# Performance work log

Hardware: AMD Instinct MI355X
Metric: run time of the kernel (lower is better)

## Reference

```python
import jax, jax.numpy as jnp
import numpy as np

LOCAL_SIZE = 20
SAMPLING_RATE = 10
LN_EPS = 1e-5


def _layer_norm(x, gamma, beta):
    m = x.mean(axis=-1, keepdims=True)
    v = ((x - m) ** 2).mean(axis=-1, keepdims=True)
    return (x - m) / jnp.sqrt(v + LN_EPS) * gamma + beta


def setup_inputs() -> dict:
    key = jax.random.key(0)
    ks = jax.random.split(key, 3)
    B, T, D, R = 32, 4096, 512, 64
    return {
        "obs_frames": jax.random.normal(ks[0], (B, T, D), dtype=jnp.float32),
        "w_red": (jax.random.normal(ks[1], (D, R), dtype=jnp.float32) / np.float32(np.sqrt(D))),
        "b_red": jnp.zeros((R,), jnp.float32),
        "g_red": jnp.ones((R,), jnp.float32),
        "beta_red": jnp.zeros((R,), jnp.float32),
        "w_exp": (jax.random.normal(ks[2], (R, D), dtype=jnp.float32) / np.float32(np.sqrt(R))),
        "b_exp": jnp.zeros((D,), jnp.float32),
        "g_exp": jnp.ones((D,), jnp.float32),
        "beta_exp": jnp.zeros((D,), jnp.float32),
    }


def reference(obs_frames, w_red, b_red, g_red, beta_red, w_exp, b_exp, g_exp, beta_exp):
    # linear_reduction: Linear -> ReLU -> LayerNorm, [B,T,D] -> [B,T,R]
    cf = _layer_norm(jax.nn.relu(jnp.einsum("btd,dr->btr", obs_frames, w_red) + b_red), g_red, beta_red)
    T = cf.shape[1]
    # max over strided past frames: indices 0, 10, ..., < T-LOCAL_SIZE
    past_pooled = jnp.max(cf[:, : T - LOCAL_SIZE : SAMPLING_RATE, :], axis=1)  # [B,R]
    # hand-rolled cummax over the last LOCAL_SIZE steps, seeded with past max
    present = cf[:, -LOCAL_SIZE:, :]                                           # [B,L,R]
    seeded = jnp.concatenate([past_pooled[:, None, :], present], axis=1)       # [B,L+1,R]
    global_reduc_max = jax.lax.associative_scan(jnp.maximum, seeded, axis=1)[:, 1:, :]  # [B,L,R]
    # _linear_expand: Linear -> ReLU -> LayerNorm, [B,L,R] -> [B,L,D]
    global_max = _layer_norm(jax.nn.relu(jnp.einsum("blr,rd->bld", global_reduc_max, w_exp) + b_exp), g_exp, beta_exp)
    now_reduc_max = cf[:, -1:, :]  # [B,1,R]
    return (global_max, now_reduc_max)
```

## Files before the change

kernel.cpp:

```cpp
#include <hip/hip_runtime.h>

static constexpr int Bsz   = 32;
static constexpr int Tlen  = 4096;
static constexpr int Ddim  = 512;
static constexpr int NSAMP = 408;
static constexpr int NPRES = 20;
static constexpr int NROWS = NSAMP + NPRES;
static constexpr int RPB   = 64;
static constexpr int NBLK  = 7;

typedef __attribute__((ext_vector_type(8))) short short8;
typedef __attribute__((ext_vector_type(4))) float f32x4;

__device__ __forceinline__ unsigned short f2bf(float x) {
  union { float f; unsigned u; } c; c.f = x;
  unsigned r = c.u + 0x7FFFu + ((c.u >> 16) & 1u);
  return (unsigned short)(r >> 16);
}

__device__ __forceinline__ int swz(int row, int colByte) {
  return (row << 10) + (colByte ^ ((row & 7) << 4));
}

__global__ __launch_bounds__(256) void k1_cf(
    const float* __restrict__ obs, const float* __restrict__ wred,
    const float* __restrict__ bred, const float* __restrict__ gred,
    const float* __restrict__ betared,
    float* __restrict__ bpart,
    float* __restrict__ present,
    float* __restrict__ out_now)
{
  __shared__ short xs[RPB * Ddim];
  __shared__ short wt[64 * Ddim];
  __shared__ float wmax[4][64];

  const int b    = blockIdx.y;
  const int bx   = blockIdx.x;
  const int base = bx * RPB;
  const int tid  = threadIdx.x;
  char* xsB = (char*)xs;
  char* wtB = (char*)wt;

  const float* obs_b = obs + (size_t)b * Tlen * Ddim;
#pragma unroll 8
  for (int it = 0; it < 32; ++it) {
    int u    = it * 256 + tid;
    int row  = u >> 7;
    int c4   = u & 127;
    int graw = base + row;
    int gr   = graw < NROWS ? graw : NROWS - 1;
    int t    = gr < NSAMP ? gr * 10 : (Tlen - NPRES) + (gr - NSAMP);
    float4 v = *(const float4*)(obs_b + (size_t)t * Ddim + c4 * 4);
    uint2 wv;
    wv.x = (unsigned)f2bf(v.x) | ((unsigned)f2bf(v.y) << 16);
    wv.y = (unsigned)f2bf(v.z) | ((unsigned)f2bf(v.w) << 16);
    *(uint2*)(xsB + swz(row, c4 * 8)) = wv;
  }

#pragma unroll 4
  for (int it = 0; it < 16; ++it) {
    int dp = it * 16 + (tid >> 4);
    int d  = dp * 2;
    int r0 = (tid & 15) * 4;
    float4 va = *(const float4*)(wred + (size_t)d * 64 + r0);
    float4 vb = *(const float4*)(wred + (size_t)(d + 1) * 64 + r0);
    *(unsigned*)(wtB + swz(r0 + 0, d * 2)) =
        (unsigned)f2bf(va.x) | ((unsigned)f2bf(vb.x) << 16);
    *(unsigned*)(wtB + swz(r0 + 1, d * 2)) =
        (unsigned)f2bf(va.y) | ((unsigned)f2bf(vb.y) << 16);
    *(unsigned*)(wtB + swz(r0 + 2, d * 2)) =
        (unsigned)f2bf(va.z) | ((unsigned)f2bf(vb.z) << 16);
    *(unsigned*)(wtB + swz(r0 + 3, d * 2)) =
        (unsigned)f2bf(va.w) | ((unsigned)f2bf(vb.w) << 16);
  }
  __syncthreads();

  const int w    = tid >> 6;
  const int lane = tid & 63;
  const int l15  = lane & 15;
  const int lhi  = lane >> 4;
  const int arow = w * 16 + l15;

  f32x4 acc0 = {0.f, 0.f, 0.f, 0.f};
  f32x4 acc1 = {0.f, 0.f, 0.f, 0.f};
  f32x4 acc2 = {0.f, 0.f, 0.f, 0.f};
  f32x4 acc3 = {0.f, 0.f, 0.f, 0.f};
#pragma unroll
  for (int ks = 0; ks < 16; ++ks) {
    int colB = ks * 64 + lhi * 16;
    short8 av  = *(const short8*)(xsB + swz(arow,     colB));
    short8 bv0 = *(const short8*)(wtB + swz(l15,      colB));
    short8 bv1 = *(const short8*)(wtB + swz(16 + l15, colB));
    short8 bv2 = *(const short8*)(wtB + swz(32 + l15, colB));
    short8 bv3 = *(const short8*)(wtB + swz(48 + l15, colB));
    acc0 = __builtin_amdgcn_mfma_f32_16x16x32_bf16(av, bv0, acc0, 0, 0, 0);
    acc1 = __builtin_amdgcn_mfma_f32_16x16x32_bf16(av, bv1, acc1, 0, 0, 0);
    acc2 = __builtin_amdgcn_mfma_f32_16x16x32_bf16(av, bv2, acc2, 0, 0, 0);
    acc3 = __builtin_amdgcn_mfma_f32_16x16x32_bf16(av, bv3, acc3, 0, 0, 0);
  }

  const int ch0 = l15, ch1 = 16 + l15, ch2 = 32 + l15, ch3 = 48 + l15;
  const float bb0 = bred[ch0], bb1 = bred[ch1], bb2 = bred[ch2], bb3 = bred[ch3];
  const float gg0 = gred[ch0], gg1 = gred[ch1], gg2 = gred[ch2], gg3 = gred[ch3];
  const float be0 = betared[ch0], be1 = betared[ch1];
  const float be2 = betared[ch2], be3 = betared[ch3];
  float m0 = -INFINITY, m1 = -INFINITY, m2 = -INFINITY, m3 = -INFINITY;
  float* pres_b = present + (size_t)b * NPRES * 64;

#pragma unroll
  for (int q = 0; q < 4; ++q) {
    int rloc = lhi * 4 + q;
    int graw = base + w * 16 + rloc;
    int gr   = graw < NROWS ? graw : NROWS - 1;
    float y0 = fmaxf(acc0[q] + bb0, 0.f);
    float y1 = fmaxf(acc1[q] + bb1, 0.f);
    float y2 = fmaxf(acc2[q] + bb2, 0.f);
    float y3 = fmaxf(acc3[q] + bb3, 0.f);
    float s  = y0 + y1 + y2 + y3;
    float s2 = y0 * y0 + y1 * y1 + y2 * y2 + y3 * y3;
#pragma unroll
    for (int msk = 1; msk <= 8; msk <<= 1) {
      s  += __shfl_xor(s,  msk, 64);
      s2 += __shfl_xor(s2, msk, 64);
    }
    float mean = s * (1.f / 64.f);
    float var  = s2 * (1.f / 64.f) - mean * mean;
    float inv  = rsqrtf(fmaxf(var, 0.f) + 1e-5f);
    float c0 = (y0 - mean) * inv * gg0 + be0;
    float c1 = (y1 - mean) * inv * gg1 + be1;
    float c2 = (y2 - mean) * inv * gg2 + be2;
    float c3 = (y3 - mean) * inv * gg3 + be3;
    if (gr < NSAMP) {
      m0 = fmaxf(m0, c0); m1 = fmaxf(m1, c1);
      m2 = fmaxf(m2, c2); m3 = fmaxf(m3, c3);
    } else {
      int l = gr - NSAMP;
      pres_b[l * 64 + ch0] = c0;  pres_b[l * 64 + ch1] = c1;
      pres_b[l * 64 + ch2] = c2;  pres_b[l * 64 + ch3] = c3;
      if (gr == NROWS - 1) {
        out_now[b * 64 + ch0] = c0;  out_now[b * 64 + ch1] = c1;
        out_now[b * 64 + ch2] = c2;  out_now[b * 64 + ch3] = c3;
      }
    }
  }

  m0 = fmaxf(m0, __shfl_xor(m0, 16, 64)); m0 = fmaxf(m0, __shfl_xor(m0, 32, 64));
  m1 = fmaxf(m1, __shfl_xor(m1, 16, 64)); m1 = fmaxf(m1, __shfl_xor(m1, 32, 64));
  m2 = fmaxf(m2, __shfl_xor(m2, 16, 64)); m2 = fmaxf(m2, __shfl_xor(m2, 32, 64));
  m3 = fmaxf(m3, __shfl_xor(m3, 16, 64)); m3 = fmaxf(m3, __shfl_xor(m3, 32, 64));
  if (lhi == 0) {
    wmax[w][ch0] = m0; wmax[w][ch1] = m1; wmax[w][ch2] = m2; wmax[w][ch3] = m3;
  }
  __syncthreads();
  if (tid < 64) {
    float m = fmaxf(fmaxf(wmax[0][tid], wmax[1][tid]),
                    fmaxf(wmax[2][tid], wmax[3][tid]));
    bpart[((size_t)b * NBLK + bx) * 64 + tid] = m;
  }
}

__global__ __launch_bounds__(256) void k3_expand(
    const float* __restrict__ wexp, const float* __restrict__ bexp,
    const float* __restrict__ gexp, const float* __restrict__ betaexp,
    const float* __restrict__ bpart, const float* __restrict__ present,
    float* __restrict__ out_gm)
{
  __shared__ float part[4][64];
  __shared__ float gm[64];
  __shared__ float red_s[4], red_s2[4];
  __shared__ float bc[2];
  const int l = blockIdx.x;
  const int b = blockIdx.y;
  const int tid = threadIdx.x;
  const int r = tid & 63, j = tid >> 6;

  const int nsrc = NBLK + l + 1;
  float v = -INFINITY;
  for (int s = j; s < nsrc; s += 4)
    v = fmaxf(v, s < NBLK ? bpart[((size_t)b * NBLK + s) * 64 + r]
                          : present[((size_t)b * NPRES + (s - NBLK)) * 64 + r]);
  part[j][r] = v;
  __syncthreads();
  if (tid < 64)
    gm[tid] = fmaxf(fmaxf(part[0][tid], part[1][tid]),
                    fmaxf(part[2][tid], part[3][tid]));
  __syncthreads();

  const int d0 = tid, d1 = tid + 256;
  float a0 = 0.f, a1 = 0.f;
#pragma unroll 8
  for (int rr = 0; rr < 64; ++rr) {
    float g = gm[rr];
    a0 = fmaf(g, wexp[rr * Ddim + d0], a0);
    a1 = fmaf(g, wexp[rr * Ddim + d1], a1);
  }
  float y0 = fmaxf(a0 + bexp[d0], 0.f);
  float y1 = fmaxf(a1 + bexp[d1], 0.f);

  float s = y0 + y1, s2 = fmaf(y0, y0, y1 * y1);
#pragma unroll
  for (int m = 32; m >= 1; m >>= 1) {
    s  += __shfl_xor(s,  m, 64);
    s2 += __shfl_xor(s2, m, 64);
  }
  int wid = tid >> 6, lane = tid & 63;
  if (lane == 0) { red_s[wid] = s; red_s2[wid] = s2; }
  __syncthreads();
  if (tid == 0) {
    float S  = red_s[0] + red_s[1] + red_s[2] + red_s[3];
    float S2 = red_s2[0] + red_s2[1] + red_s2[2] + red_s2[3];
    float mean = S * (1.f / 512.f);
    float var  = S2 * (1.f / 512.f) - mean * mean;
    bc[0] = mean;
    bc[1] = rsqrtf(fmaxf(var, 0.f) + 1e-5f);
  }
  __syncthreads();
  float mean = bc[0], inv = bc[1];
  size_t o = ((size_t)b * NPRES + l) * Ddim;
  out_gm[o + d0] = (y0 - mean) * inv * gexp[d0] + betaexp[d0];
  out_gm[o + d1] = (y1 - mean) * inv * gexp[d1] + betaexp[d1];
}

extern "C" void kernel_launch(void* const* d_in, const int* in_sizes, int n_in,
                              void* d_out, int out_size, void* d_ws, size_t ws_size,
                              hipStream_t stream) {
  const float* obs     = (const float*)d_in[0];
  const float* wred    = (const float*)d_in[1];
  const float* bred    = (const float*)d_in[2];
  const float* gred    = (const float*)d_in[3];
  const float* betared = (const float*)d_in[4];
  const float* wexp    = (const float*)d_in[5];
  const float* bexp    = (const float*)d_in[6];
  const float* gexp    = (const float*)d_in[7];
  const float* betaexp = (const float*)d_in[8];

  float* out_gm  = (float*)d_out;
  float* out_now = (float*)d_out + Bsz * NPRES * Ddim;

  float* bpart   = (float*)d_ws;
  float* present = bpart + Bsz * NBLK * 64;

  dim3 g1(NBLK, Bsz);
  k1_cf<<<g1, 256, 0, stream>>>(obs, wred, bred, gred, betared,
                                bpart, present, out_now);

  dim3 g3(NPRES, Bsz);
  k3_expand<<<g3, 256, 0, stream>>>(wexp, bexp, gexp, betaexp,
                                    bpart, present, out_gm);
}
```

Before: 26.38 us.

## Widen reduction kernel to 1024 threads and fuse two output rows per expand block

The first kernel now launches 1024 threads per block. Each of its 16 waves computes one 16x16 MFMA tile, split by row group and channel group, instead of 4 waves each computing four tiles. LayerNorm statistics are then combined across waves through shared memory, which adds a barrier. The aim is more memory-level parallelism for the strided gather of input frames, since only 224 blocks run. The expand kernel now handles two output time steps per block, reusing each loaded w_exp value for both rows and halving the grid.

```diff
diff --git a/kernel.cpp b/kernel.cpp
--- a/kernel.cpp
+++ b/kernel.cpp
@@ -22,7 +22,7 @@
   return (row << 10) + (colByte ^ ((row & 7) << 4));
 }
 
-__global__ __launch_bounds__(256) void k1_cf(
+__global__ __launch_bounds__(1024) void k1_cf(
     const float* __restrict__ obs, const float* __restrict__ wred,
     const float* __restrict__ bred, const float* __restrict__ gred,
     const float* __restrict__ betared,
@@ -32,6 +32,8 @@
 {
   __shared__ short xs[RPB * Ddim];
   __shared__ short wt[64 * Ddim];
+  __shared__ float sred[64][4];
+  __shared__ float s2red[64][4];
   __shared__ float wmax[4][64];
 
   const int b    = blockIdx.y;
@@ -42,9 +44,9 @@
   char* wtB = (char*)wt;
 
   const float* obs_b = obs + (size_t)b * Tlen * Ddim;
-#pragma unroll 8
-  for (int it = 0; it < 32; ++it) {
-    int u    = it * 256 + tid;
+#pragma unroll
+  for (int it = 0; it < 8; ++it) {
+    int u    = it * 1024 + tid;
     int row  = u >> 7;
     int c4   = u & 127;
     int graw = base + row;
@@ -57,9 +59,9 @@
     *(uint2*)(xsB + swz(row, c4 * 8)) = wv;
   }
 
-#pragma unroll 4
-  for (int it = 0; it < 16; ++it) {
-    int dp = it * 16 + (tid >> 4);
+#pragma unroll
+  for (int it = 0; it < 4; ++it) {
+    int dp = it * 64 + (tid >> 4);
     int d  = dp * 2;
     int r0 = (tid & 15) * 4;
     float4 va = *(const float4*)(wred + (size_t)d * 64 + r0);
@@ -79,83 +81,70 @@
   const int lane = tid & 63;
   const int l15  = lane & 15;
   const int lhi  = lane >> 4;
-  const int arow = w * 16 + l15;
-
-  f32x4 acc0 = {0.f, 0.f, 0.f, 0.f};
-  f32x4 acc1 = {0.f, 0.f, 0.f, 0.f};
-  f32x4 acc2 = {0.f, 0.f, 0.f, 0.f};
-  f32x4 acc3 = {0.f, 0.f, 0.f, 0.f};
+  const int rowg = w & 3;
+  const int chg  = w >> 2;
+  const int arow = rowg * 16 + l15;
+  const int brow = chg * 16 + l15;
+
+  f32x4 acc = {0.f, 0.f, 0.f, 0.f};
 #pragma unroll
   for (int ks = 0; ks < 16; ++ks) {
     int colB = ks * 64 + lhi * 16;
-    short8 av  = *(const short8*)(xsB + swz(arow,     colB));
-    short8 bv0 = *(const short8*)(wtB + swz(l15,      colB));
-    short8 bv1 = *(const short8*)(wtB + swz(16 + l15, colB));
-    short8 bv2 = *(const short8*)(wtB + swz(32 + l15, colB));
-    short8 bv3 = *(const short8*)(wtB + swz(48 + l15, colB));
-    acc0 = __builtin_amdgcn_mfma_f32_16x16x32_bf16(av, bv0, acc0, 0, 0, 0);
-    acc1 = __builtin_amdgcn_mfma_f32_16x16x32_bf16(av, bv1, acc1, 0, 0, 0);
-    acc2 = __builtin_amdgcn_mfma_f32_16x16x32_bf16(av, bv2, acc2, 0, 0, 0);
-    acc3 = __builtin_amdgcn_mfma_f32_16x16x32_bf16(av, bv3, acc3, 0, 0, 0);
-  }
-
-  const int ch0 = l15, ch1 = 16 + l15, ch2 = 32 + l15, ch3 = 48 + l15;
-  const float bb0 = bred[ch0], bb1 = bred[ch1], bb2 = bred[ch2], bb3 = bred[ch3];
-  const float gg0 = gred[ch0], gg1 = gred[ch1], gg2 = gred[ch2], gg3 = gred[ch3];
-  const float be0 = betared[ch0], be1 = betared[ch1];
-  const float be2 = betared[ch2], be3 = betared[ch3];
-  float m0 = -INFINITY, m1 = -INFINITY, m2 = -INFINITY, m3 = -INFINITY;
-  float* pres_b = present + (size_t)b * NPRES * 64;
-
+    short8 av = *(const short8*)(xsB + swz(arow, colB));
+    short8 bv = *(const short8*)(wtB + swz(brow, colB));
+    acc = __builtin_amdgcn_mfma_f32_16x16x32_bf16(av, bv, acc, 0, 0, 0);
+  }
+
+  const int c  = chg * 16 + l15;
+  const float bb = bred[c], gg = gred[c], be = betared[c];
+  float y[4];
 #pragma unroll
   for (int q = 0; q < 4; ++q) {
-    int rloc = lhi * 4 + q;
-    int graw = base + w * 16 + rloc;
-    int gr   = graw < NROWS ? graw : NROWS - 1;
-    float y0 = fmaxf(acc0[q] + bb0, 0.f);
-    float y1 = fmaxf(acc1[q] + bb1, 0.f);
-    float y2 = fmaxf(acc2[q] + bb2, 0.f);
-    float y3 = fmaxf(acc3[q] + bb3, 0.f);
-    float s  = y0 + y1 + y2 + y3;
-    float s2 = y0 * y0 + y1 * y1 + y2 * y2 + y3 * y3;
+    y[q] = fmaxf(acc[q] + bb, 0.f);
+    float s = y[q], s2 = y[q] * y[q];
 #pragma unroll
     for (int msk = 1; msk <= 8; msk <<= 1) {
       s  += __shfl_xor(s,  msk, 64);
       s2 += __shfl_xor(s2, msk, 64);
     }
-    float mean = s * (1.f / 64.f);
-    float var  = s2 * (1.f / 64.f) - mean * mean;
+    if (l15 == 0) {
+      int grow = rowg * 16 + lhi * 4 + q;
+      sred[grow][chg]  = s;
+      s2red[grow][chg] = s2;
+    }
+  }
+  __syncthreads();
+
+  float m = -INFINITY;
+  float* pres_b = present + (size_t)b * NPRES * 64;
+#pragma unroll
+  for (int q = 0; q < 4; ++q) {
+    int grow = rowg * 16 + lhi * 4 + q;
+    float S  = sred[grow][0] + sred[grow][1] + sred[grow][2] + sred[grow][3];
+    float S2 = s2red[grow][0] + s2red[grow][1] + s2red[grow][2] + s2red[grow][3];
+    float mean = S * (1.f / 64.f);
+    float var  = S2 * (1.f / 64.f) - mean * mean;
     float inv  = rsqrtf(fmaxf(var, 0.f) + 1e-5f);
-    float c0 = (y0 - mean) * inv * gg0 + be0;
-    float c1 = (y1 - mean) * inv * gg1 + be1;
-    float c2 = (y2 - mean) * inv * gg2 + be2;
-    float c3 = (y3 - mean) * inv * gg3 + be3;
+    float cf   = (y[q] - mean) * inv * gg + be;
+    int graw = base + grow;
+    int gr   = graw < NROWS ? graw : NROWS - 1;
     if (gr < NSAMP) {
-      m0 = fmaxf(m0, c0); m1 = fmaxf(m1, c1);
-      m2 = fmaxf(m2, c2); m3 = fmaxf(m3, c3);
+      m = fmaxf(m, cf);
     } else {
       int l = gr - NSAMP;
-      pres_b[l * 64 + ch0] = c0;  pres_b[l * 64 + ch1] = c1;
-      pres_b[l * 64 + ch2] = c2;  pres_b[l * 64 + ch3] = c3;
-      if (gr == NROWS - 1) {
-        out_now[b * 64 + ch0] = c0;  out_now[b * 64 + ch1] = c1;
-        out_now[b * 64 + ch2] = c2;  out_now[b * 64 + ch3] = c3;
-      }
-    }
-  }
-
-  m0 = fmaxf(m0, __shfl_xor(m0, 16, 64)); m0 = fmaxf(m0, __shfl_xor(m0, 32, 64));
-  m1 = fmaxf(m1, __shfl_xor(m1, 16, 64)); m1 = fmaxf(m1, __shfl_xor(m1, 32, 64));
-  m2 = fmaxf(m2, __shfl_xor(m2, 16, 64)); m2 = fmaxf(m2, __shfl_xor(m2, 32, 64));
-  m3 = fmaxf(m3, __shfl_xor(m3, 16, 64)); m3 = fmaxf(m3, __shfl_xor(m3, 32, 64));
-  if (lhi == 0) {
-    wmax[w][ch0] = m0; wmax[w][ch1] = m1; wmax[w][ch2] = m2; wmax[w][ch3] = m3;
-  }
+      pres_b[l * 64 + c] = cf;
+      if (gr == NROWS - 1) out_now[b * 64 + c] = cf;
+    }
+  }
+
+  m = fmaxf(m, __shfl_xor(m, 16, 64));
+  m = fmaxf(m, __shfl_xor(m, 32, 64));
+  if (lhi == 0) wmax[rowg][c] = m;
   __syncthreads();
   if (tid < 64) {
-    float m = fmaxf(fmaxf(wmax[0][tid], wmax[1][tid]),
-                    fmaxf(wmax[2][tid], wmax[3][tid]));
-    bpart[((size_t)b * NBLK + bx) * 64 + tid] = m;
+    float mm = fmaxf(fmaxf(wmax[0][tid], wmax[1][tid]),
+                     fmaxf(wmax[2][tid], wmax[3][tid]));
+    bpart[((size_t)b * NBLK + bx) * 64 + tid] = mm;
   }
 }
 
@@ -165,60 +154,85 @@
     const float* __restrict__ bpart, const float* __restrict__ present,
     float* __restrict__ out_gm)
 {
-  __shared__ float part[4][64];
-  __shared__ float gm[64];
-  __shared__ float red_s[4], red_s2[4];
-  __shared__ float bc[2];
-  const int l = blockIdx.x;
-  const int b = blockIdx.y;
+  __shared__ float partA[4][64], partB[4][64];
+  __shared__ float gm0[64], gm1[64];
+  __shared__ float red_s[2][4], red_s2[2][4];
+  __shared__ float bc[2][2];
+  const int l0 = blockIdx.x * 2, l1 = l0 + 1;
+  const int b  = blockIdx.y;
   const int tid = threadIdx.x;
   const int r = tid & 63, j = tid >> 6;
 
-  const int nsrc = NBLK + l + 1;
-  float v = -INFINITY;
-  for (int s = j; s < nsrc; s += 4)
-    v = fmaxf(v, s < NBLK ? bpart[((size_t)b * NBLK + s) * 64 + r]
-                          : present[((size_t)b * NPRES + (s - NBLK)) * 64 + r]);
-  part[j][r] = v;
-  __syncthreads();
-  if (tid < 64)
-    gm[tid] = fmaxf(fmaxf(part[0][tid], part[1][tid]),
-                    fmaxf(part[2][tid], part[3][tid]));
+  const int n0 = NBLK + l0 + 1;
+  const int n1 = n0 + 1;
+  float vA = -INFINITY, vB = -INFINITY;
+  for (int s = j; s < n1; s += 4) {
+    float x = s < NBLK ? bpart[((size_t)b * NBLK + s) * 64 + r]
+                       : present[((size_t)b * NPRES + (s - NBLK)) * 64 + r];
+    vB = fmaxf(vB, x);
+    if (s < n0) vA = fmaxf(vA, x);
+  }
+  partA[j][r] = vA;
+  partB[j][r] = vB;
+  __syncthreads();
+  if (tid < 64) {
+    gm0[tid] = fmaxf(fmaxf(partA[0][tid], partA[1][tid]),
+                     fmaxf(partA[2][tid], partA[3][tid]));
+  } else if (tid < 128) {
+    int t = tid - 64;
+    gm1[t] = fmaxf(fmaxf(partB[0][t], partB[1][t]),
+                   fmaxf(partB[2][t], partB[3][t]));
+  }
   __syncthreads();
 
   const int d0 = tid, d1 = tid + 256;
-  float a0 = 0.f, a1 = 0.f;
+  float a00 = 0.f, a01 = 0.f, a10 = 0.f, a11 = 0.f;
 #pragma unroll 8
   for (int rr = 0; rr < 64; ++rr) {
-    float g = gm[rr];
-    a0 = fmaf(g, wexp[rr * Ddim + d0], a0);
-    a1 = fmaf(g, wexp[rr * Ddim + d1], a1);
-  }
-  float y0 = fmaxf(a0 + bexp[d0], 0.f);
-  float y1 = fmaxf(a1 + bexp[d1], 0.f);
-
-  float s = y0 + y1, s2 = fmaf(y0, y0, y1 * y1);
-#pragma unroll
-  for (int m = 32; m >= 1; m >>= 1) {
-    s  += __shfl_xor(s,  m, 64);
-    s2 += __shfl_xor(s2, m, 64);
+    float g0 = gm0[rr], g1 = gm1[rr];
+    float w0 = wexp[rr * Ddim + d0], w1 = wexp[rr * Ddim + d1];
+    a00 = fmaf(g0, w0, a00);  a01 = fmaf(g0, w1, a01);
+    a10 = fmaf(g1, w0, a10);  a11 = fmaf(g1, w1, a11);
+  }
+  const float bx0 = bexp[d0], bx1 = bexp[d1];
+  float y00 = fmaxf(a00 + bx0, 0.f), y01 = fmaxf(a01 + bx1, 0.f);
+  float y10 = fmaxf(a10 + bx0, 0.f), y11 = fmaxf(a11 + bx1, 0.f);
+
+  float s0 = y00 + y01, s20 = fmaf(y00, y00, y01 * y01);
+  float s1 = y10 + y11, s21 = fmaf(y10, y10, y11 * y11);
+#pragma unroll
+  for (int msk = 32; msk >= 1; msk >>= 1) {
+    s0  += __shfl_xor(s0,  msk, 64);
+    s20 += __shfl_xor(s20, msk, 64);
+    s1  += __shfl_xor(s1,  msk, 64);
+    s21 += __shfl_xor(s21, msk, 64);
   }
   int wid = tid >> 6, lane = tid & 63;
-  if (lane == 0) { red_s[wid] = s; red_s2[wid] = s2; }
+  if (lane == 0) {
+    red_s[0][wid] = s0;  red_s2[0][wid] = s20;
+    red_s[1][wid] = s1;  red_s2[1][wid] = s21;
+  }
   __syncthreads();
   if (tid == 0) {
-    float S  = red_s[0] + red_s[1] + red_s[2] + red_s[3];
-    float S2 = red_s2[0] + red_s2[1] + red_s2[2] + red_s2[3];
-    float mean = S * (1.f / 512.f);
-    float var  = S2 * (1.f / 512.f) - mean * mean;
-    bc[0] = mean;
-    bc[1] = rsqrtf(fmaxf(var, 0.f) + 1e-5f);
-  }
-  __syncthreads();
-  float mean = bc[0], inv = bc[1];
-  size_t o = ((size_t)b * NPRES + l) * Ddim;
-  out_gm[o + d0] = (y0 - mean) * inv * gexp[d0] + betaexp[d0];
-  out_gm[o + d1] = (y1 - mean) * inv * gexp[d1] + betaexp[d1];
+#pragma unroll
+    for (int ll = 0; ll < 2; ++ll) {
+      float S  = red_s[ll][0] + red_s[ll][1] + red_s[ll][2] + red_s[ll][3];
+      float S2 = red_s2[ll][0] + red_s2[ll][1] + red_s2[ll][2] + red_s2[ll][3];
+      float mean = S * (1.f / 512.f);
+      float var  = S2 * (1.f / 512.f) - mean * mean;
+      bc[ll][0] = mean;
+      bc[ll][1] = rsqrtf(fmaxf(var, 0.f) + 1e-5f);
+    }
+  }
+  __syncthreads();
+  const float g0c = gexp[d0], g1c = gexp[d1];
+  const float be0 = betaexp[d0], be1 = betaexp[d1];
+  size_t o0 = ((size_t)b * NPRES + l0) * Ddim;
+  size_t o1 = ((size_t)b * NPRES + l1) * Ddim;
+  out_gm[o0 + d0] = (y00 - bc[0][0]) * bc[0][1] * g0c + be0;
+  out_gm[o0 + d1] = (y01 - bc[0][0]) * bc[0][1] * g1c + be1;
+  out_gm[o1 + d0] = (y10 - bc[1][0]) * bc[1][1] * g0c + be0;
+  out_gm[o1 + d1] = (y11 - bc[1][0]) * bc[1][1] * g1c + be1;
 }
 
 extern "C" void kernel_launch(void* const* d_in, const int* in_sizes, int n_in,
@@ -241,10 +255,10 @@
   float* present = bpart + Bsz * NBLK * 64;
 
   dim3 g1(NBLK, Bsz);
-  k1_cf<<<g1, 256, 0, stream>>>(obs, wred, bred, gred, betared,
-                                bpart, present, out_now);
-
-  dim3 g3(NPRES, Bsz);
+  k1_cf<<<g1, 1024, 0, stream>>>(obs, wred, bred, gred, betared,
+                                 bpart, present, out_now);
+
+  dim3 g3(NPRES / 2, Bsz);
   k3_expand<<<g3, 256, 0, stream>>>(wexp, bexp, gexp, betaexp,
                                     bpart, present, out_gm);
 }
```

Result: faster. 22.31 us (-15.4%).

## Prepack reduction weight once, use 1024-thread blocks splitting channels across waves

Applied to the files above, without the earlier changes.

Adds a small pre-kernel that converts w_red to bf16 in transposed layout in the workspace, so each block no longer converts the whole weight into shared memory. The main kernel now runs 1024 threads with 16 waves, each computing one 16x16 output tile and reading B fragments straight from global/L2. LayerNorm statistics are reduced across channel groups through shared memory, which adds a barrier. This trades redundant per-block weight conversion and shared-memory staging for an extra launch and global-memory B loads.

```diff
diff --git a/kernel.cpp b/kernel.cpp
--- a/kernel.cpp
+++ b/kernel.cpp
@@ -22,8 +22,21 @@
   return (row << 10) + (colByte ^ ((row & 7) << 4));
 }
 
-__global__ __launch_bounds__(256) void k1_cf(
-    const float* __restrict__ obs, const float* __restrict__ wred,
+__global__ __launch_bounds__(256) void k0_pack(
+    const float* __restrict__ wred, unsigned short* __restrict__ wt_g)
+{
+  int t  = blockIdx.x * 256 + threadIdx.x;
+  int kg = t >> 6;
+  int ch = t & 63;
+  int k0 = kg * 2;
+  float a = wred[(size_t)k0 * 64 + ch];
+  float b = wred[(size_t)(k0 + 1) * 64 + ch];
+  unsigned pack = (unsigned)f2bf(a) | ((unsigned)f2bf(b) << 16);
+  *(unsigned*)(wt_g + (size_t)ch * Ddim + k0) = pack;
+}
+
+__global__ __launch_bounds__(1024, 8) void k1_cf(
+    const float* __restrict__ obs, const unsigned short* __restrict__ wt_g,
     const float* __restrict__ bred, const float* __restrict__ gred,
     const float* __restrict__ betared,
     float* __restrict__ bpart,
@@ -31,7 +44,8 @@
     float* __restrict__ out_now)
 {
   __shared__ short xs[RPB * Ddim];
-  __shared__ short wt[64 * Ddim];
+  __shared__ float sred[64][4];
+  __shared__ float s2red[64][4];
   __shared__ float wmax[4][64];
 
   const int b    = blockIdx.y;
@@ -39,12 +53,11 @@
   const int base = bx * RPB;
   const int tid  = threadIdx.x;
   char* xsB = (char*)xs;
-  char* wtB = (char*)wt;
 
   const float* obs_b = obs + (size_t)b * Tlen * Ddim;
-#pragma unroll 8
-  for (int it = 0; it < 32; ++it) {
-    int u    = it * 256 + tid;
+#pragma unroll
+  for (int it = 0; it < 8; ++it) {
+    int u    = it * 1024 + tid;
     int row  = u >> 7;
     int c4   = u & 127;
     int graw = base + row;
@@ -56,110 +69,81 @@
     wv.y = (unsigned)f2bf(v.z) | ((unsigned)f2bf(v.w) << 16);
     *(uint2*)(xsB + swz(row, c4 * 8)) = wv;
   }
-
-#pragma unroll 4
-  for (int it = 0; it < 16; ++it) {
-    int dp = it * 16 + (tid >> 4);
-    int d  = dp * 2;
-    int r0 = (tid & 15) * 4;
-    float4 va = *(const float4*)(wred + (size_t)d * 64 + r0);
-    float4 vb = *(const float4*)(wred + (size_t)(d + 1) * 64 + r0);
-    *(unsigned*)(wtB + swz(r0 + 0, d * 2)) =
-        (unsigned)f2bf(va.x) | ((unsigned)f2bf(vb.x) << 16);
-    *(unsigned*)(wtB + swz(r0 + 1, d * 2)) =
-        (unsigned)f2bf(va.y) | ((unsigned)f2bf(vb.y) << 16);
-    *(unsigned*)(wtB + swz(r0 + 2, d * 2)) =
-        (unsigned)f2bf(va.z) | ((unsigned)f2bf(vb.z) << 16);
-    *(unsigned*)(wtB + swz(r0 + 3, d * 2)) =
-        (unsigned)f2bf(va.w) | ((unsigned)f2bf(vb.w) << 16);
-  }
   __syncthreads();
 
   const int w    = tid >> 6;
   const int lane = tid & 63;
   const int l15  = lane & 15;
   const int lhi  = lane >> 4;
-  const int arow = w * 16 + l15;
-
-  f32x4 acc0 = {0.f, 0.f, 0.f, 0.f};
-  f32x4 acc1 = {0.f, 0.f, 0.f, 0.f};
-  f32x4 acc2 = {0.f, 0.f, 0.f, 0.f};
-  f32x4 acc3 = {0.f, 0.f, 0.f, 0.f};
+  const int rowg = w & 3;
+  const int chg  = w >> 2;
+  const int arow = rowg * 16 + l15;
+  const int brow = chg * 16 + l15;
+  const char* wrow = (const char*)(wt_g + (size_t)brow * Ddim);
+
+  f32x4 acc = {0.f, 0.f, 0.f, 0.f};
 #pragma unroll
   for (int ks = 0; ks < 16; ++ks) {
     int colB = ks * 64 + lhi * 16;
-    short8 av  = *(const short8*)(xsB + swz(arow,     colB));
-    short8 bv0 = *(const short8*)(wtB + swz(l15,      colB));
-    short8 bv1 = *(const short8*)(wtB + swz(16 + l15, colB));
-    short8 bv2 = *(const short8*)(wtB + swz(32 + l15, colB));
-    short8 bv3 = *(const short8*)(wtB + swz(48 + l15, colB));
-    acc0 = __builtin_amdgcn_mfma_f32_16x16x32_bf16(av, bv0, acc0, 0, 0, 0);
-    acc1 = __builtin_amdgcn_mfma_f32_16x16x32_bf16(av, bv1, acc1, 0, 0, 0);
-    acc2 = __builtin_amdgcn_mfma_f32_16x16x32_bf16(av, bv2, acc2, 0, 0, 0);
-    acc3 = __builtin_amdgcn_mfma_f32_16x16x32_bf16(av, bv3, acc3, 0, 0, 0);
-  }
-
-  const int ch0 = l15, ch1 = 16 + l15, ch2 = 32 + l15, ch3 = 48 + l15;
-  const float bb0 = bred[ch0], bb1 = bred[ch1], bb2 = bred[ch2], bb3 = bred[ch3];
-  const float gg0 = gred[ch0], gg1 = gred[ch1], gg2 = gred[ch2], gg3 = gred[ch3];
-  const float be0 = betared[ch0], be1 = betared[ch1];
-  const float be2 = betared[ch2], be3 = betared[ch3];
-  float m0 = -INFINITY, m1 = -INFINITY, m2 = -INFINITY, m3 = -INFINITY;
-  float* pres_b = present + (size_t)b * NPRES * 64;
-
+    short8 av = *(const short8*)(xsB + swz(arow, colB));
+    short8 bv = *(const short8*)(wrow + colB);
+    acc = __builtin_amdgcn_mfma_f32_16x16x32_bf16(av, bv, acc, 0, 0, 0);
+  }
+
+  const int c  = chg * 16 + l15;
+  const float bb = bred[c], gg = gred[c], be = betared[c];
+  float y[4];
 #pragma unroll
   for (int q = 0; q < 4; ++q) {
-    int rloc = lhi * 4 + q;
-    int graw = base + w * 16 + rloc;
-    int gr   = graw < NROWS ? graw : NROWS - 1;
-    float y0 = fmaxf(acc0[q] + bb0, 0.f);
-    float y1 = fmaxf(acc1[q] + bb1, 0.f);
-    float y2 = fmaxf(acc2[q] + bb2, 0.f);
-    float y3 = fmaxf(acc3[q] + bb3, 0.f);
-    float s  = y0 + y1 + y2 + y3;
-    float s2 = y0 * y0 + y1 * y1 + y2 * y2 + y3 * y3;
+    y[q] = fmaxf(acc[q] + bb, 0.f);
+    float s = y[q], s2 = y[q] * y[q];
 #pragma unroll
     for (int msk = 1; msk <= 8; msk <<= 1) {
       s  += __shfl_xor(s,  msk, 64);
       s2 += __shfl_xor(s2, msk, 64);
     }
-    float mean = s * (1.f / 64.f);
-    float var  = s2 * (1.f / 64.f) - mean * mean;
+    if (l15 == 0) {
+      int grow = rowg * 16 + lhi * 4 + q;
+      sred[grow][chg]  = s;
+      s2red[grow][chg] = s2;
+    }
+  }
+  __syncthreads();
+
+  float m = -INFINITY;
+  float* pres_b = present + (size_t)b * NPRES * 64;
+#pragma unroll
+  for (int q = 0; q < 4; ++q) {
+    int grow = rowg * 16 + lhi * 4 + q;
+    float S  = sred[grow][0] + sred[grow][1] + sred[grow][2] + sred[grow][3];
+    float S2 = s2red[grow][0] + s2red[grow][1] + s2red[grow][2] + s2red[grow][3];
+    float mean = S * (1.f / 64.f);
+    float var  = S2 * (1.f / 64.f) - mean * mean;
     float inv  = rsqrtf(fmaxf(var, 0.f) + 1e-5f);
-    float c0 = (y0 - mean) * inv * gg0 + be0;
-    float c1 = (y1 - mean) * inv * gg1 + be1;
-    float c2 = (y2 - mean) * inv * gg2 + be2;
-    float c3 = (y3 - mean) * inv * gg3 + be3;
+    float cf   = (y[q] - mean) * inv * gg + be;
+    int graw = base + grow;
+    int gr   = graw < NROWS ? graw : NROWS - 1;
     if (gr < NSAMP) {
-      m0 = fmaxf(m0, c0); m1 = fmaxf(m1, c1);
-      m2 = fmaxf(m2, c2); m3 = fmaxf(m3, c3);
+      m = fmaxf(m, cf);
     } else {
       int l = gr - NSAMP;
-      pres_b[l * 64 + ch0] = c0;  pres_b[l * 64 + ch1] = c1;
-      pres_b[l * 64 + ch2] = c2;  pres_b[l * 64 + ch3] = c3;
-      if (gr == NROWS - 1) {
-        out_now[b * 64 + ch0] = c0;  out_now[b * 64 + ch1] = c1;
-        out_now[b * 64 + ch2] = c2;  out_now[b * 64 + ch3] = c3;
-      }
+      pres_b[l * 64 + c] = cf;
+      if (gr == NROWS - 1) out_now[b * 64 + c] = cf;
     }
   }
 
-  m0 = fmaxf(m0, __shfl_xor(m0, 16, 64)); m0 = fmaxf(m0, __shfl_xor(m0, 32, 64));
-  m1 = fmaxf(m1, __shfl_xor(m1, 16, 64)); m1 = fmaxf(m1, __shfl_xor(m1, 32, 64));
-  m2 = fmaxf(m2, __shfl_xor(m2, 16, 64)); m2 = fmaxf(m2, __shfl_xor(m2, 32, 64));
-  m3 = fmaxf(m3, __shfl_xor(m3, 16, 64)); m3 = fmaxf(m3, __shfl_xor(m3, 32, 64));
-  if (lhi == 0) {
-    wmax[w][ch0] = m0; wmax[w][ch1] = m1; wmax[w][ch2] = m2; wmax[w][ch3] = m3;
-  }
+  m = fmaxf(m, __shfl_xor(m, 16, 64));
+  m = fmaxf(m, __shfl_xor(m, 32, 64));
+  if (lhi == 0) wmax[rowg][c] = m;
   __syncthreads();
   if (tid < 64) {
-    float m = fmaxf(fmaxf(wmax[0][tid], wmax[1][tid]),
-                    fmaxf(wmax[2][tid], wmax[3][tid]));
-    bpart[((size_t)b * NBLK + bx) * 64 + tid] = m;
-  }
-}
-
-__global__ __launch_bounds__(256) void k3_expand(
+    float mm = fmaxf(fmaxf(wmax[0][tid], wmax[1][tid]),
+                     fmaxf(wmax[2][tid], wmax[3][tid]));
+    bpart[((size_t)b * NBLK + bx) * 64 + tid] = mm;
+  }
+}
+
+__global__ __launch_bounds__(256, 8) void k3_expand(
     const float* __restrict__ wexp, const float* __restrict__ bexp,
     const float* __restrict__ gexp, const float* __restrict__ betaexp,
     const float* __restrict__ bpart, const float* __restrict__ present,
@@ -237,12 +221,15 @@
   float* out_gm  = (float*)d_out;
   float* out_now = (float*)d_out + Bsz * NPRES * Ddim;
 
-  float* bpart   = (float*)d_ws;
+  unsigned short* wt_g = (unsigned short*)d_ws;
+  float* bpart   = (float*)((char*)d_ws + 64 * Ddim * sizeof(short));
   float* present = bpart + Bsz * NBLK * 64;
 
+  k0_pack<<<64, 256, 0, stream>>>(wred, wt_g);
+
   dim3 g1(NBLK, Bsz);
-  k1_cf<<<g1, 256, 0, stream>>>(obs, wred, bred, gred, betared,
-                                bpart, present, out_now);
+  k1_cf<<<g1, 1024, 0, stream>>>(obs, wt_g, bred, gred, betared,
+                                 bpart, present, out_now);
 
   dim3 g3(NPRES, Bsz);
   k3_expand<<<g3, 256, 0, stream>>>(wexp, bexp, gexp, betaexp,
```

Result: slower. 30.41 us (+15.3%).
